# Performance work log

Hardware: AMD Instinct MI355X
Metric: run time of the kernel (lower is better)

## Reference

```python
import jax, jax.numpy as jnp
import numpy as np

# ---- static config (LCNN wirenet) ----
K = 128            # fixed junction count per type (n_dyn_junc // n_type)
N_PTS0 = 32
N_PTS1 = 8
SCALE = N_PTS0 // N_PTS1   # maxpool1d kernel/stride = 4
DIM_LOI = 128
DIM_FC = 1024
FEATURE_DIM = 8
USE_COOD = 0.0
USE_SLOP = 0.0
HW = 128
B = 2
# static u<v pair indices (torch: meshgrid -> c = u < v), P = K*(K-1)/2
IU_np, IV_np = np.triu_indices(K, k=1)
P = IU_np.shape[0]
IU = jnp.asarray(IU_np, jnp.int32)
IV = jnp.asarray(IV_np, jnp.int32)
LAMBDA = jnp.linspace(0.0, 1.0, N_PTS0)[:, None]  # [32,1]


def setup_inputs() -> dict:
    key = jax.random.key(0)
    ks = jax.random.split(key, 8)
    inputs = jax.random.normal(ks[0], (B, 5, HW, HW), jnp.float32)
    features = jax.random.normal(ks[1], (B, 256, HW, HW), jnp.float32)
    fc1_w = jax.random.normal(ks[2], (DIM_LOI, 256), jnp.float32) * 0.05
    fc1_b = jnp.zeros((DIM_LOI,), jnp.float32)
    d_in = DIM_LOI * N_PTS1 + FEATURE_DIM  # 1032
    w1 = jax.random.normal(ks[3], (d_in, DIM_FC), jnp.float32) * 0.03
    b1 = jnp.zeros((DIM_FC,), jnp.float32)
    w2 = jax.random.normal(ks[4], (DIM_FC, DIM_FC), jnp.float32) * 0.03
    b2 = jnp.zeros((DIM_FC,), jnp.float32)
    w3 = jax.random.normal(ks[5], (DIM_FC, 1), jnp.float32) * 0.03
    b3 = jnp.zeros((1,), jnp.float32)
    return dict(inputs=inputs, features=features, fc1_w=fc1_w, fc1_b=fc1_b,
                w1=w1, b1=b1, w2=w2, b2=b2, w3=w3, b3=b3)


def _nms(a):
    # a: [1,H,W]; 3x3 max-pool NMS, keep only local maxima
    ap = jax.lax.reduce_window(a, -jnp.inf, jax.lax.max, (1, 3, 3), (1, 1, 1), 'SAME')
    return a * (a == ap).astype(a.dtype)


def _sample_lines(jmap, joff):
    # jmap: [1,H,W], joff: [1,2,H,W]  (inference path: dummy junc/Lpos)
    n_type = 1
    jm = _nms(jmap).reshape(n_type, -1)            # [1, HW*HW]
    jo = joff.reshape(n_type, 2, -1)
    score, index = jax.lax.top_k(jm, K)            # [1,K]
    y = (index // HW).astype(jnp.float32) + jnp.take_along_axis(jo[:, 0], index, 1) + 0.5
    x = (index % HW).astype(jnp.float32) + jnp.take_along_axis(jo[:, 1], index, 1) + 0.5
    xy = jnp.stack([y, x], -1)                     # [1,K,2]
    # inference dummies: junc=zeros(1,2), jtyp=zeros(1), Lpos=zeros(2,2)
    junc = jnp.zeros((1, 2), jnp.float32)
    jtyp = jnp.zeros((1,), jnp.int32)
    dist = jnp.sum((xy[:, :, None, :] - junc) ** 2, -1)  # [1,K,1]
    cost = jnp.min(dist, -1)
    match = jnp.argmin(dist, -1).astype(jnp.int32)       # [1,K]
    Njunc = 1
    match = jnp.where(jtyp[match] != jnp.arange(n_type, dtype=jnp.int32)[:, None], Njunc, match)
    match = jnp.where(cost > 1.5 * 1.5, Njunc, match).reshape(-1)  # [K]
    up, vp = match[IU], match[IV]
    Lpos = jnp.zeros((2, 2), jnp.float32)
    label = Lpos[up, vp]                           # [P]
    xyf = xy.reshape(n_type * K, 2)
    xyu, xyv = xyf[IU], xyf[IV]                    # [P,2]
    u2v = xyu - xyv
    u2v = u2v / jnp.clip(jnp.sqrt(jnp.sum(u2v ** 2, -1, keepdims=True)), 1e-6)
    feat = jnp.concatenate([
        xyu / HW * USE_COOD, xyv / HW * USE_COOD, u2v * USE_SLOP,
        (IU[:, None] > K).astype(jnp.float32), (IV[:, None] > K).astype(jnp.float32)], 1)  # [P,8]
    line = jnp.stack([xyu, xyv], 1)                # [P,2,2]
    return line, label, feat


def _loi_pool(xfeat, line):
    # xfeat: [C,H,W], line: [P,2,2] -> [P,C,N_PTS1]
    p = line[:, 0:1, :] * LAMBDA + line[:, 1:2, :] * (1.0 - LAMBDA) - 0.5  # [P,32,2]
    p = p.reshape(-1, 2)
    px, py = p[:, 0], p[:, 1]
    px0 = jnp.clip(jnp.floor(px), 0, HW - 1)
    py0 = jnp.clip(jnp.floor(py), 0, HW - 1)
    px1 = jnp.clip(px0 + 1, 0, HW - 1)
    py1 = jnp.clip(py0 + 1, 0, HW - 1)
    px0l = px0.astype(jnp.int32); py0l = py0.astype(jnp.int32)
    px1l = px1.astype(jnp.int32); py1l = py1.astype(jnp.int32)
    xp = (xfeat[:, px0l, py0l] * (px1 - px) * (py1 - py)
          + xfeat[:, px1l, py0l] * (px - px0) * (py1 - py)
          + xfeat[:, px0l, py1l] * (px1 - px) * (py - py0)
          + xfeat[:, px1l, py1l] * (px - px0) * (py - py0))  # [C, P*32]
    xp = xp.reshape(DIM_LOI, -1, N_PTS0).transpose(1, 0, 2)  # [P,C,32]
    # MaxPool1d(kernel=4, stride=4)
    return xp.reshape(xp.shape[0], DIM_LOI, N_PTS1, SCALE).max(-1)  # [P,C,8]


def _forward(inputs, features, fc1_w, fc1_b, w1, b1, w2, b2, w3, b3):
    b, _, r, c = inputs.shape
    out = jnp.transpose(inputs, (1, 0, 2, 3))       # [5,B,H,W]
    jmap_logits = out[0:2].reshape(1, 2, b, r, c)
    joff_logits = out[3:5].reshape(1, 2, b, r, c)
    jmap = jax.nn.softmax(jnp.transpose(jmap_logits, (2, 0, 1, 3, 4)), axis=2)[:, :, 1]  # [B,1,H,W]
    joff = jax.nn.sigmoid(jnp.transpose(joff_logits, (2, 0, 1, 3, 4))) - 0.5             # [B,1,2,H,W]
    # fc1: 1x1 conv 256 -> dim_loi
    xf = jnp.einsum('bchw,dc->bdhw', features, fc1_w) + fc1_b[None, :, None, None]
    lines, labels, feats = jax.vmap(_sample_lines)(jmap, joff)   # [B,P,2,2],[B,P],[B,P,8]
    # sample_lines runs under torch.no_grad()
    lines = jax.lax.stop_gradient(lines)
    labels = jax.lax.stop_gradient(labels)
    feats = jax.lax.stop_gradient(feats)
    xp = jax.vmap(_loi_pool)(xf, lines)             # [B,P,C,8]
    xv = xp.reshape(-1, N_PTS1 * DIM_LOI)           # [B*P, 1024] (C-major then pts)
    xv = jnp.concatenate([xv, feats.reshape(-1, FEATURE_DIM)], 1)  # [B*P, 1032]
    h = jax.nn.relu(xv @ w1 + b1)
    h = jax.nn.relu(h @ w2 + b2)
    scores = (h @ w3 + b3).reshape(-1)              # [B*P]
    return scores, labels.reshape(-1), lines


def reference(inputs, features, fc1_w, fc1_b, w1, b1, w2, b2, w3, b3):
    return _forward(inputs, features, fc1_w, fc1_b, w1, b1, w2, b2, w3, b3)
```

## Files before the change

kernel.cpp:

```cpp
#include <hip/hip_runtime.h>
#include <hip/hip_bf16.h>
#include <math.h>

#define HW 128
#define NPIX 16384
#define KTOP 128
#define PPAIR 8128
#define NB 2
#define DIMLOI 128
#define NROWS (NB*PPAIR)
#define MPAD 16384

typedef __bf16 bf16x8 __attribute__((ext_vector_type(8)));
typedef float floatx4 __attribute__((ext_vector_type(4)));
typedef float floatx8 __attribute__((ext_vector_type(8)));

__device__ __forceinline__ unsigned long long mk_key(float v, int idx) {
    return ((unsigned long long)__float_as_uint(v) << 32) |
           (unsigned long long)(0xFFFFFFFFu - (unsigned)idx);
}

__device__ __forceinline__ unsigned long long shfl_xor_u64(unsigned long long x, int m) {
    unsigned lo = (unsigned)x, hi = (unsigned)(x >> 32);
    lo = __shfl_xor(lo, m);
    hi = __shfl_xor(hi, m);
    return ((unsigned long long)hi << 32) | lo;
}

__device__ __forceinline__ void bitonic_stage(unsigned long long V[4], int lane, int j, int k) {
    if (j >= 64) {
        int qm = j >> 6;
        #pragma unroll
        for (int q = 0; q < 4; q++) {
            int p = q ^ qm;
            if (p > q) {
                int i = q * 64 + lane;
                bool desc = ((i & k) == 0);
                unsigned long long a = V[q], b = V[p];
                unsigned long long hi = a > b ? a : b, lo = a > b ? b : a;
                V[q] = desc ? hi : lo;
                V[p] = desc ? lo : hi;
            }
        }
    } else {
        #pragma unroll
        for (int q = 0; q < 4; q++) {
            int i = q * 64 + lane;
            unsigned long long p = shfl_xor_u64(V[q], j);
            bool lower = (lane & j) == 0;
            bool desc = ((i & k) == 0);
            bool keepmax = (desc == lower);
            unsigned long long mx = V[q] > p ? V[q] : p;
            unsigned long long mn = V[q] > p ? p : V[q];
            V[q] = keepmax ? mx : mn;
        }
    }
}

__device__ __forceinline__ void sort256_desc(unsigned long long V[4], int lane) {
    #pragma unroll
    for (int k = 2; k <= 256; k <<= 1)
        #pragma unroll
        for (int j = k >> 1; j >= 1; j >>= 1)
            bitonic_stage(V, lane, j, k);
}

__device__ __forceinline__ void merge256_desc(unsigned long long V[4], int lane) {
    #pragma unroll
    for (int j = 128; j >= 1; j >>= 1)
        bitonic_stage(V, lane, j, 256);
}

__global__ __launch_bounds__(256) void nms_sort_kernel(const float* __restrict__ inp,
                                                       unsigned long long* __restrict__ tkeys) {
    __shared__ float jm[10 * HW];
    __shared__ unsigned long long cand[256];
    __shared__ int scnt;
    int blk = blockIdx.x;
    int b   = blockIdx.y;
    int tid = threadIdx.x, lane = tid & 63;
    int r0  = blk * 8;
    int rlo = (r0 > 0) ? r0 - 1 : 0;
    int rhi = (r0 + 8 < HW) ? r0 + 8 : HW - 1;
    int nrows = rhi - rlo + 1;

    for (int i = tid; i < nrows * HW; i += 256) {
        int pix = rlo * HW + i;
        float l0 = inp[((long)b * 5 + 0) * NPIX + pix];
        float l1 = inp[((long)b * 5 + 1) * NPIX + pix];
        float m = fmaxf(l0, l1);
        float e0 = expf(l0 - m), e1 = expf(l1 - m);
        jm[i] = e1 / (e0 + e1);
    }
    cand[tid] = 0ull;
    if (tid == 0) scnt = 0;
    __syncthreads();

    #pragma unroll
    for (int i = 0; i < 4; i++) {
        int pl = i * 256 + tid;
        int r = r0 + (pl >> 7), c = pl & 127;
        float v = jm[(r - rlo) * HW + c];
        float m = v;
        for (int dr = -1; dr <= 1; dr++) {
            int rr = r + dr;
            if (rr < 0 || rr >= HW) continue;
            for (int dc = -1; dc <= 1; dc++) {
                int cc = c + dc;
                if (cc < 0 || cc >= HW) continue;
                m = fmaxf(m, jm[(rr - rlo) * HW + cc]);
            }
        }
        float nv = (v == m) ? v : 0.f;
        bool has = (nv > 0.f);
        unsigned long long mask = __ballot(has);
        int n = __popcll(mask);
        int wbase = 0;
        if (lane == 0 && n) wbase = atomicAdd(&scnt, n);
        wbase = __shfl(wbase, 0);
        if (has) {
            int pos = wbase + __popcll(mask & ((1ull << lane) - 1ull));
            if (pos < 256) cand[pos] = mk_key(nv, r * HW + c);
        }
    }
    __syncthreads();
    if (blk == 0 && tid < 128 && tid >= scnt) cand[tid] = mk_key(0.f, tid);
    __syncthreads();

    if (tid < 64) {
        unsigned long long V[4];
        #pragma unroll
        for (int q = 0; q < 4; q++) V[q] = cand[q * 64 + lane];
        sort256_desc(V, lane);
        #pragma unroll
        for (int q = 0; q < 2; q++)
            tkeys[((long)b * 16 + blk) * 128 + q * 64 + lane] = V[q];
    }
}

__global__ __launch_bounds__(512) void topk_merge_kernel(const unsigned long long* __restrict__ tkeys,
                                                         const float* __restrict__ inp,
                                                         float* __restrict__ xy) {
    __shared__ unsigned long long Lb[16 * 128];
    __shared__ unsigned long long Mb[8 * 128];
    int b = blockIdx.x;
    int tid = threadIdx.x, w = tid >> 6, lane = tid & 63;
    for (int i = tid; i < 16 * 128; i += 512) Lb[i] = tkeys[(long)b * 2048 + i];
    __syncthreads();

    unsigned long long* src = Lb;
    unsigned long long* dst = Mb;
    for (int nact = 8; nact >= 1; nact >>= 1) {
        unsigned long long V[4];
        if (w < nact) {
            #pragma unroll
            for (int q = 0; q < 2; q++) V[q] = src[(2 * w) * 128 + q * 64 + lane];
            #pragma unroll
            for (int q = 2; q < 4; q++) {
                int t = (q - 2) * 64 + lane;
                V[q] = src[(2 * w + 1) * 128 + 127 - t];
            }
            merge256_desc(V, lane);
        }
        __syncthreads();
        if (w < nact) {
            #pragma unroll
            for (int q = 0; q < 2; q++) dst[w * 128 + q * 64 + lane] = V[q];
        }
        __syncthreads();
        unsigned long long* tmp = src; src = dst; dst = tmp;
    }

    if (tid < KTOP) {
        unsigned long long key = src[tid];
        int wi = (int)(0xFFFFFFFFu - (unsigned)(key & 0xFFFFFFFFull));
        int row = wi >> 7, col = wi & 127;
        float l3 = inp[((long)b * 5 + 3) * NPIX + wi];
        float l4 = inp[((long)b * 5 + 4) * NPIX + wi];
        float joy = 1.f / (1.f + expf(-l3)) - 0.5f;
        float jox = 1.f / (1.f + expf(-l4)) - 0.5f;
        xy[(b * KTOP + tid) * 2 + 0] = (float)row + joy + 0.5f;
        xy[(b * KTOP + tid) * 2 + 1] = (float)col + jox + 0.5f;
    }
}

__device__ __forceinline__ void pair_uv(int p, int& u, int& v) {
    int uu = (int)((255.0 - sqrt(65025.0 - 8.0 * (double)p)) * 0.5);
    if (uu < 0) uu = 0;
    while (uu * (255 - uu) / 2 > p) uu--;
    while ((uu + 1) * (255 - (uu + 1)) / 2 <= p) uu++;
    u = uu;
    v = uu + 1 + (p - uu * (255 - uu) / 2);
}

__global__ void lines_kernel(const float* __restrict__ xy, float* __restrict__ out) {
    int r = blockIdx.x * 256 + threadIdx.x;
    if (r >= NROWS) return;
    int b = r / PPAIR, p = r % PPAIR;
    int u, v; pair_uv(p, u, v);
    float yu = xy[(b * KTOP + u) * 2 + 0], xu = xy[(b * KTOP + u) * 2 + 1];
    float yv = xy[(b * KTOP + v) * 2 + 0], xv = xy[(b * KTOP + v) * 2 + 1];
    float* lines = out + 2 * NROWS;
    long base = (long)r * 4;
    lines[base + 0] = yu; lines[base + 1] = xu;
    lines[base + 2] = yv; lines[base + 3] = xv;
    out[NROWS + r] = 0.f;
}

__global__ void prep_weights(const float* __restrict__ w1, const float* __restrict__ w2,
                             const float* __restrict__ fc1w,
                             __hip_bfloat16* __restrict__ w1t, __hip_bfloat16* __restrict__ w2t,
                             __hip_bfloat16* __restrict__ fc1wb) {
    int z = blockIdx.z;
    int tx = threadIdx.x & 31, ty = threadIdx.x >> 5;
    if (z < 2) {
        const float* W = z ? w2 : w1;
        __hip_bfloat16* Wt = z ? w2t : w1t;
        __shared__ float t[32][33];
        int k0 = blockIdx.x * 32, n0 = blockIdx.y * 32;
        #pragma unroll
        for (int i = 0; i < 32; i += 8)
            t[ty + i][tx] = W[(long)(k0 + ty + i) * 1024 + n0 + tx];
        __syncthreads();
        #pragma unroll
        for (int i = 0; i < 32; i += 8)
            Wt[(long)(n0 + ty + i) * 1024 + k0 + tx] = __float2bfloat16(t[tx][ty + i]);
    } else {
        if (blockIdx.x < 4 && blockIdx.y < 8) {
            int r0 = blockIdx.x * 32, c0 = blockIdx.y * 32;
            #pragma unroll
            for (int i = 0; i < 32; i += 8) {
                long idx = (long)(r0 + ty + i) * 256 + c0 + tx;
                fc1wb[idx] = __float2bfloat16(fc1w[idx]);
            }
        }
    }
}

__device__ __forceinline__ void gload_lds16(const void* g, void* l) {
    __builtin_amdgcn_global_load_lds(
        (const __attribute__((address_space(1))) void*)g,
        (__attribute__((address_space(3))) void*)l, 16, 0, 0);
}

#define SA 264

__global__ __launch_bounds__(256) void xf_fused_kernel(
    const float* __restrict__ features, const __hip_bfloat16* __restrict__ fc1wb,
    const float* __restrict__ bias, __hip_bfloat16* __restrict__ C0) {
    __shared__ __align__(16) __bf16 A_lds[128 * SA];
    __shared__ __align__(16) unsigned short B_lds[128 * 32 * 8];
    int tid = threadIdx.x;
    int lane = tid & 63, wid = tid >> 6;
    int wr = wid >> 1, wc = wid & 1;
    int b = blockIdx.z;
    long pix0 = (long)blockIdx.x * 128;

    #pragma unroll
    for (int it = 0; it < 16; it++) {
        int slot = it * 256 + tid;
        int r = slot >> 5, s = slot & 31;
        int ss = s ^ (r & 7);
        gload_lds16(fc1wb + (size_t)r * 256 + ss * 8,
                    (char*)B_lds + (size_t)(it * 4096 + wid * 1024));
    }
    {
        int c = tid;
        const float* src = features + ((long)b * 256 + c) * NPIX + pix0;
        #pragma unroll
        for (int p4 = 0; p4 < 32; p4++) {
            floatx4 v = *(const floatx4*)(src + p4 * 4);
            #pragma unroll
            for (int e = 0; e < 4; e++)
                A_lds[(p4 * 4 + e) * SA + c] = (__bf16)v[e];
        }
    }
    __syncthreads();

    floatx4 acc[4][4];
    #pragma unroll
    for (int i = 0; i < 4; i++)
        #pragma unroll
        for (int j = 0; j < 4; j++) acc[i][j] = (floatx4){0.f, 0.f, 0.f, 0.f};

    int r15 = lane & 15;
    #pragma unroll
    for (int ks = 0; ks < 8; ks++) {
        int s = (lane >> 4) + ks * 4;
        bf16x8 af[4], bfr[4];
        #pragma unroll
        for (int mi = 0; mi < 4; mi++) {
            int R = wr * 64 + mi * 16 + r15;
            af[mi] = *(const bf16x8*)&A_lds[R * SA + s * 8];
        }
        #pragma unroll
        for (int ni = 0; ni < 4; ni++) {
            int Rn = wc * 64 + ni * 16 + r15;
            bfr[ni] = *(const bf16x8*)&B_lds[(size_t)Rn * 256 + ((s ^ (Rn & 7)) << 3)];
        }
        #pragma unroll
        for (int mi = 0; mi < 4; mi++)
            #pragma unroll
            for (int ni = 0; ni < 4; ni++)
                acc[mi][ni] = __builtin_amdgcn_mfma_f32_16x16x32_bf16(
                    af[mi], bfr[ni], acc[mi][ni], 0, 0, 0);
    }

    __hip_bfloat16* C = C0 + (long)b * NPIX * DIMLOI;
    #pragma unroll
    for (int ni = 0; ni < 4; ni++) {
        long c = wc * 64 + ni * 16 + r15;
        float bv = bias[c];
        #pragma unroll
        for (int mi = 0; mi < 4; mi++) {
            long rbase = pix0 + wr * 64 + mi * 16 + (lane >> 4) * 4;
            #pragma unroll
            for (int q = 0; q < 4; q++)
                C[(rbase + q) * (long)DIMLOI + c] = __float2bfloat16(acc[mi][ni][q] + bv);
        }
    }
}

#define BM 128
#define BN 128
#define BKK 64

template <bool SCORE>
__global__ __launch_bounds__(256) void gemm_mfma(
    const __hip_bfloat16* __restrict__ A, const __hip_bfloat16* __restrict__ Bt,
    const float* __restrict__ bias, __hip_bfloat16* __restrict__ C,
    int M, int N, int Kd,
    const float* __restrict__ w3, float* __restrict__ slab) {
    int bid = blockIdx.x;
    int xcd = bid & 7, j = bid >> 3;
    int mtpx = (M / BM) >> 3;
    int mt = xcd * mtpx + (j >> 3);
    int nt = j & 7;
    long row0 = (long)mt * BM, col0 = (long)nt * BN;

    __shared__ __align__(16) unsigned short As[BM * BKK];
    __shared__ __align__(16) unsigned short Bs[BN * BKK];
    int tid = threadIdx.x;
    int lane = tid & 63, wid = tid >> 6;
    int wr = wid >> 1, wc = wid & 1;

    floatx4 acc[4][4];
    #pragma unroll
    for (int i = 0; i < 4; i++)
        #pragma unroll
        for (int jj = 0; jj < 4; jj++) acc[i][jj] = (floatx4){0.f, 0.f, 0.f, 0.f};

    for (int k0 = 0; k0 < Kd; k0 += BKK) {
        #pragma unroll
        for (int it = 0; it < 4; it++) {
            int slot = wid * 256 + it * 64 + lane;
            int r = slot >> 3, s = slot & 7;
            int ss = s ^ (r & 7);
            gload_lds16(A + (row0 + r) * Kd + k0 + ss * 8,
                        (char*)As + (size_t)(wid * 4096 + it * 1024));
        }
        #pragma unroll
        for (int it = 0; it < 4; it++) {
            int slot = wid * 256 + it * 64 + lane;
            int r = slot >> 3, s = slot & 7;
            int ss = s ^ (r & 7);
            gload_lds16(Bt + (col0 + r) * Kd + k0 + ss * 8,
                        (char*)Bs + (size_t)(wid * 4096 + it * 1024));
        }
        __syncthreads();
        #pragma unroll
        for (int ks = 0; ks < 2; ks++) {
            bf16x8 af[4], bfr[4];
            int s = (lane >> 4) + ks * 4;
            #pragma unroll
            for (int mi = 0; mi < 4; mi++) {
                int R = wr * 64 + mi * 16 + (lane & 15);
                af[mi] = *(const bf16x8*)&As[R * BKK + ((s ^ (R & 7)) << 3)];
            }
            #pragma unroll
            for (int ni = 0; ni < 4; ni++) {
                int Rn = wc * 64 + ni * 16 + (lane & 15);
                bfr[ni] = *(const bf16x8*)&Bs[Rn * BKK + ((s ^ (Rn & 7)) << 3)];
            }
            #pragma unroll
            for (int mi = 0; mi < 4; mi++)
                #pragma unroll
                for (int ni = 0; ni < 4; ni++)
                    acc[mi][ni] = __builtin_amdgcn_mfma_f32_16x16x32_bf16(
                        af[mi], bfr[ni], acc[mi][ni], 0, 0, 0);
        }
        __syncthreads();
    }

    if constexpr (SCORE) {
        int ntile = (int)(col0 / BN);
        #pragma unroll
        for (int mi = 0; mi < 4; mi++) {
            #pragma unroll
            for (int q = 0; q < 4; q++) {
                float p = 0.f;
                #pragma unroll
                for (int ni = 0; ni < 4; ni++) {
                    long c = col0 + wc * 64 + ni * 16 + (lane & 15);
                    float v = fmaxf(acc[mi][ni][q] + bias[c], 0.f);
                    p += v * w3[c];
                }
                #pragma unroll
                for (int off = 1; off < 16; off <<= 1) p += __shfl_xor(p, off);
                if ((lane & 15) == 0) {
                    long row = row0 + wr * 64 + mi * 16 + (lane >> 4) * 4 + q;
                    slab[(long)(ntile * 2 + wc) * MPAD + row] = p;
                }
            }
        }
    } else {
        #pragma unroll
        for (int ni = 0; ni < 4; ni++) {
            long c = col0 + wc * 64 + ni * 16 + (lane & 15);
            float bv = bias[c];
            #pragma unroll
            for (int mi = 0; mi < 4; mi++) {
                long rbase = row0 + wr * 64 + mi * 16 + (lane >> 4) * 4;
                #pragma unroll
                for (int q = 0; q < 4; q++) {
                    float v = fmaxf(acc[mi][ni][q] + bv, 0.f);
                    C[(rbase + q) * (long)N + c] = __float2bfloat16(v);
                }
            }
        }
    }
}

__global__ void score_reduce_kernel(const float* __restrict__ slab, const float* __restrict__ b3,
                                    float* __restrict__ out) {
    int r = blockIdx.x * 256 + threadIdx.x;
    if (r >= NROWS) return;
    float s = b3[0];
    #pragma unroll
    for (int i = 0; i < 16; i++) s += slab[(long)i * MPAD + r];
    out[r] = s;
}

__global__ __launch_bounds__(256) void loi_sample_kernel(
    const __hip_bfloat16* __restrict__ xf, const float* __restrict__ xy,
    __hip_bfloat16* __restrict__ xp) {
    __shared__ int md[16 * 32 * 8];
    int tid = threadIdx.x;
    int bid = blockIdx.x;
    int swz = (bid & 7) * 128 + (bid >> 3);
    int rbase = swz * 16;

    {
        int pt0 = tid * 2;
        int sub = pt0 >> 5;
        int r = rbase + sub;
        int rm = (r < NROWS) ? r : NROWS - 1;
        int b = rm / PPAIR, p = rm % PPAIR;
        int u, v; pair_uv(p, u, v);
        float yu = xy[(b * KTOP + u) * 2 + 0], xu = xy[(b * KTOP + u) * 2 + 1];
        float yv = xy[(b * KTOP + v) * 2 + 0], xv = xy[(b * KTOP + v) * 2 + 1];
        #pragma unroll
        for (int pp = 0; pp < 2; pp++) {
            int t = (pt0 + pp) & 31;
            float lam = (float)t * (1.0f / 31.0f);
            float px = yu * lam + yv * (1.f - lam) - 0.5f;
            float py = xu * lam + xv * (1.f - lam) - 0.5f;
            float px0 = fminf(fmaxf(floorf(px), 0.f), 127.f);
            float py0 = fminf(fmaxf(floorf(py), 0.f), 127.f);
            float px1 = fminf(px0 + 1.f, 127.f);
            float py1 = fminf(py0 + 1.f, 127.f);
            int ix0 = (int)px0, iy0 = (int)py0, ix1 = (int)px1, iy1 = (int)py1;
            int base = (pt0 + pp) * 8;
            md[base + 0] = (ix0 * HW + iy0) * (DIMLOI * 2);
            md[base + 1] = (ix1 * HW + iy0) * (DIMLOI * 2);
            md[base + 2] = (ix0 * HW + iy1) * (DIMLOI * 2);
            md[base + 3] = (ix1 * HW + iy1) * (DIMLOI * 2);
            md[base + 4] = __float_as_int((px1 - px) * (py1 - py));
            md[base + 5] = __float_as_int((px - px0) * (py1 - py));
            md[base + 6] = __float_as_int((px1 - px) * (py - py0));
            md[base + 7] = __float_as_int((px - px0) * (py - py0));
        }
    }
    __syncthreads();

    int sub2 = tid >> 4, o = tid & 15;
    int r = rbase + sub2;
    int rm = (r < NROWS) ? r : NROWS - 1;
    int b = rm / PPAIR;
    const char* xfb = (const char*)(xf + (long)b * NPIX * DIMLOI) + o * 16;
    floatx8 mx[8];
    #pragma unroll
    for (int q = 0; q < 8; q++)
        #pragma unroll
        for (int e = 0; e < 8; e++) mx[q][e] = -INFINITY;
    #pragma unroll
    for (int tt = 0; tt < 32; tt++) {
        const int* m = &md[(sub2 * 32 + tt) * 8];
        bf16x8 v00 = *(const bf16x8*)(xfb + m[0]);
        bf16x8 v10 = *(const bf16x8*)(xfb + m[1]);
        bf16x8 v01 = *(const bf16x8*)(xfb + m[2]);
        bf16x8 v11 = *(const bf16x8*)(xfb + m[3]);
        float w00 = __int_as_float(m[4]), w10 = __int_as_float(m[5]);
        float w01 = __int_as_float(m[6]), w11 = __int_as_float(m[7]);
        floatx8 s;
        #pragma unroll
        for (int e = 0; e < 8; e++)
            s[e] = (float)v00[e] * w00 + (float)v10[e] * w10 +
                   (float)v01[e] * w01 + (float)v11[e] * w11;
        mx[tt >> 2] = __builtin_elementwise_max(mx[tt >> 2], s);
    }
    __hip_bfloat16* rowp = xp + (long)r * 1024 + o * 64;
    #pragma unroll
    for (int e = 0; e < 8; e++) {
        bf16x8 outv;
        #pragma unroll
        for (int q = 0; q < 8; q++) outv[q] = (__bf16)mx[q][e];
        *(bf16x8*)(rowp + e * 8) = outv;
    }
}

extern "C" void kernel_launch(void* const* d_in, const int* in_sizes, int n_in,
                              void* d_out, int out_size, void* d_ws, size_t ws_size,
                              hipStream_t stream) {
    const float* inputs   = (const float*)d_in[0];
    const float* features = (const float*)d_in[1];
    const float* fc1_w    = (const float*)d_in[2];
    const float* fc1_b    = (const float*)d_in[3];
    const float* w1       = (const float*)d_in[4];
    const float* b1       = (const float*)d_in[5];
    const float* w2       = (const float*)d_in[6];
    const float* b2       = (const float*)d_in[7];
    const float* w3       = (const float*)d_in[8];
    const float* b3       = (const float*)d_in[9];
    float* out = (float*)d_out;
    float* ws  = (float*)d_ws;

    float* xy   = ws + 65536;
    __hip_bfloat16* xfb16 = (__hip_bfloat16*)(ws + 66048);
    __hip_bfloat16* xp    = (__hip_bfloat16*)(ws + 4260352);
    __hip_bfloat16* h1    = (__hip_bfloat16*)(ws + 12648960);
    float* slab           = ws + 21037568;
    __hip_bfloat16* w1t   = (__hip_bfloat16*)(ws + 21299712);
    __hip_bfloat16* w2t   = (__hip_bfloat16*)(ws + 21824000);
    __hip_bfloat16* fc1wb = (__hip_bfloat16*)(ws + 22348288);
    unsigned long long* tkeys = (unsigned long long*)(ws + 22364672);

    prep_weights<<<dim3(32, 32, 3), 256, 0, stream>>>(w1, w2, fc1_w, w1t, w2t, fc1wb);

    nms_sort_kernel<<<dim3(16, NB), 256, 0, stream>>>(inputs, tkeys);
    topk_merge_kernel<<<NB, 512, 0, stream>>>(tkeys, inputs, xy);
    lines_kernel<<<(NROWS + 255) / 256, 256, 0, stream>>>(xy, out);

    xf_fused_kernel<<<dim3(NPIX / 128, 1, NB), 256, 0, stream>>>(
        features, fc1wb, fc1_b, xfb16);

    loi_sample_kernel<<<MPAD / 16, 256, 0, stream>>>(xfb16, xy, xp);

    gemm_mfma<false><<<(MPAD / BM) * 8, 256, 0, stream>>>(
        xp, w1t, b1, h1, MPAD, 1024, 1024, nullptr, nullptr);
    gemm_mfma<true><<<(MPAD / BM) * 8, 256, 0, stream>>>(
        h1, w2t, b2, nullptr, MPAD, 1024, 1024, w3, slab);
    score_reduce_kernel<<<(NROWS + 255) / 256, 256, 0, stream>>>(slab, b3, out);
}
```

Measured before the change: 167.5 us.

## Rewrite MLP GEMMs as 256x256-tile 8-wave kernels with double-buffered LDS pipeline

The two MLP GEMMs move from 128x128 tiles with 4 waves to 256x256 tiles with 8 waves. LDS staging is now double-buffered, with the A and B loads issued one and two k-steps ahead and interleaved with MFMA phases under explicit vmcnt waits, barriers and setprio. The goal is to hide global-to-LDS latency and cut global traffic per FLOP through more operand reuse. In exchange the kernel uses more registers and LDS, launches only 256 blocks, and hard-codes M/N/K to 1024, so occupancy and load balance may suffer.

```diff
diff --git a/kernel.cpp b/kernel.cpp
--- a/kernel.cpp
+++ b/kernel.cpp
@@ -321,110 +321,136 @@
     }
 }
 
-#define BM 128
-#define BN 128
-#define BKK 64
+#define NT16 16
 
 template <bool SCORE>
-__global__ __launch_bounds__(256) void gemm_mfma(
+__global__ __launch_bounds__(512, 2) void gemm_mlp8(
     const __hip_bfloat16* __restrict__ A, const __hip_bfloat16* __restrict__ Bt,
     const float* __restrict__ bias, __hip_bfloat16* __restrict__ C,
-    int M, int N, int Kd,
     const float* __restrict__ w3, float* __restrict__ slab) {
+    __shared__ __align__(128) unsigned short As[2][2][128][8][8];
+    __shared__ __align__(128) unsigned short Bs[2][2][128][8][8];
+    int tid = threadIdx.x;
+    int lane = tid & 63, wid = tid >> 6;
+    int wr = wid >> 2, wn = wid & 3;
+    int r15 = lane & 15, s4 = lane >> 4;
     int bid = blockIdx.x;
     int xcd = bid & 7, j = bid >> 3;
-    int mtpx = (M / BM) >> 3;
-    int mt = xcd * mtpx + (j >> 3);
-    int nt = j & 7;
-    long row0 = (long)mt * BM, col0 = (long)nt * BN;
-
-    __shared__ __align__(16) unsigned short As[BM * BKK];
-    __shared__ __align__(16) unsigned short Bs[BN * BKK];
-    int tid = threadIdx.x;
-    int lane = tid & 63, wid = tid >> 6;
-    int wr = wid >> 1, wc = wid & 1;
-
-    floatx4 acc[4][4];
-    #pragma unroll
-    for (int i = 0; i < 4; i++)
-        #pragma unroll
-        for (int jj = 0; jj < 4; jj++) acc[i][jj] = (floatx4){0.f, 0.f, 0.f, 0.f};
-
-    for (int k0 = 0; k0 < Kd; k0 += BKK) {
-        #pragma unroll
-        for (int it = 0; it < 4; it++) {
-            int slot = wid * 256 + it * 64 + lane;
-            int r = slot >> 3, s = slot & 7;
-            int ss = s ^ (r & 7);
-            gload_lds16(A + (row0 + r) * Kd + k0 + ss * 8,
-                        (char*)As + (size_t)(wid * 4096 + it * 1024));
-        }
-        #pragma unroll
-        for (int it = 0; it < 4; it++) {
-            int slot = wid * 256 + it * 64 + lane;
-            int r = slot >> 3, s = slot & 7;
-            int ss = s ^ (r & 7);
-            gload_lds16(Bt + (col0 + r) * Kd + k0 + ss * 8,
-                        (char*)Bs + (size_t)(wid * 4096 + it * 1024));
-        }
-        __syncthreads();
-        #pragma unroll
-        for (int ks = 0; ks < 2; ks++) {
-            bf16x8 af[4], bfr[4];
-            int s = (lane >> 4) + ks * 4;
-            #pragma unroll
-            for (int mi = 0; mi < 4; mi++) {
-                int R = wr * 64 + mi * 16 + (lane & 15);
-                af[mi] = *(const bf16x8*)&As[R * BKK + ((s ^ (R & 7)) << 3)];
-            }
-            #pragma unroll
-            for (int ni = 0; ni < 4; ni++) {
-                int Rn = wc * 64 + ni * 16 + (lane & 15);
-                bfr[ni] = *(const bf16x8*)&Bs[Rn * BKK + ((s ^ (Rn & 7)) << 3)];
-            }
-            #pragma unroll
-            for (int mi = 0; mi < 4; mi++)
+    int mt = xcd * 8 + (j >> 2), nt = j & 3;
+    long row0 = (long)mt * 256, col0 = (long)nt * 256;
+
+    auto stageA = [&](int tk, int h) {
+        int bf = tk & 1;
+        #pragma unroll
+        for (int it = 0; it < 2; it++) {
+            int sl = it * 512 + tid;
+            int r = sl >> 3, s = sl & 7;
+            gload_lds16(A + (row0 + h * 128 + r) * 1024 + tk * 64 + ((s ^ (r & 7)) << 3),
+                        (char*)&As[bf][h][0][0][0] + (size_t)sl * 16);
+        }
+    };
+    auto stageB = [&](int tk, int h) {
+        int bf = tk & 1;
+        #pragma unroll
+        for (int it = 0; it < 2; it++) {
+            int sl = it * 512 + tid;
+            int r = sl >> 3, s = sl & 7;
+            gload_lds16(Bt + (col0 + h * 128 + r) * 1024 + tk * 64 + ((s ^ (r & 7)) << 3),
+                        (char*)&Bs[bf][h][0][0][0] + (size_t)sl * 16);
+        }
+    };
+
+    floatx4 acc[8][4];
+    #pragma unroll
+    for (int mi = 0; mi < 8; mi++)
+        #pragma unroll
+        for (int nf = 0; nf < 4; nf++) acc[mi][nf] = (floatx4){0.f, 0.f, 0.f, 0.f};
+
+    stageA(0, 0); stageA(0, 1); stageB(0, 0); stageB(0, 1); stageB(1, 0); stageB(1, 1);
+    asm volatile("s_waitcnt vmcnt(4)" ::: "memory");
+    __builtin_amdgcn_s_barrier();
+
+    for (int t = 0; t < NT16; t++) {
+        int bf = t & 1;
+        bf16x8 bfr[4][2];
+        #pragma unroll
+        for (int p = 0; p < 4; p++) {
+            if (p == 0) {
                 #pragma unroll
-                for (int ni = 0; ni < 4; ni++)
-                    acc[mi][ni] = __builtin_amdgcn_mfma_f32_16x16x32_bf16(
-                        af[mi], bfr[ni], acc[mi][ni], 0, 0, 0);
-        }
-        __syncthreads();
+                for (int nf = 0; nf < 4; nf++)
+                    #pragma unroll
+                    for (int ks = 0; ks < 2; ks++) {
+                        int Rb = wn * 64 + nf * 16 + r15;
+                        int rh = Rb & 127;
+                        bfr[nf][ks] = *(const bf16x8*)&Bs[bf][Rb >> 7][rh][(ks * 4 + s4) ^ (rh & 7)][0];
+                    }
+            }
+            bf16x8 af[2][2];
+            #pragma unroll
+            for (int m = 0; m < 2; m++)
+                #pragma unroll
+                for (int ks = 0; ks < 2; ks++) {
+                    int rh = (2 * p + m) * 16 + r15;
+                    af[m][ks] = *(const bf16x8*)&As[bf][wr][rh][(ks * 4 + s4) ^ (rh & 7)][0];
+                }
+            if (p == 0) { if (t + 1 < NT16) stageA(t + 1, 0); }
+            else if (p == 1) { if (t + 1 < NT16) stageA(t + 1, 1); }
+            else if (p == 2) { if (t + 2 < NT16) stageB(t + 2, 0); }
+            else             { if (t + 2 < NT16) stageB(t + 2, 1); }
+            if (p == 3) {
+                if (t < NT16 - 2) { asm volatile("s_waitcnt vmcnt(4)" ::: "memory"); }
+                else              { asm volatile("s_waitcnt vmcnt(0)" ::: "memory"); }
+            }
+            __builtin_amdgcn_s_barrier();
+            asm volatile("s_waitcnt lgkmcnt(0)" ::: "memory");
+            __builtin_amdgcn_sched_barrier(0);
+            __builtin_amdgcn_s_setprio(1);
+            #pragma unroll
+            for (int m = 0; m < 2; m++)
+                #pragma unroll
+                for (int nf = 0; nf < 4; nf++)
+                    #pragma unroll
+                    for (int ks = 0; ks < 2; ks++)
+                        acc[2 * p + m][nf] = __builtin_amdgcn_mfma_f32_16x16x32_bf16(
+                            af[m][ks], bfr[nf][ks], acc[2 * p + m][nf], 0, 0, 0);
+            __builtin_amdgcn_s_setprio(0);
+            __builtin_amdgcn_s_barrier();
+        }
     }
 
     if constexpr (SCORE) {
-        int ntile = (int)(col0 / BN);
-        #pragma unroll
-        for (int mi = 0; mi < 4; mi++) {
+        int slot = nt * 4 + wn;
+        #pragma unroll
+        for (int mi = 0; mi < 8; mi++) {
             #pragma unroll
             for (int q = 0; q < 4; q++) {
                 float p = 0.f;
                 #pragma unroll
-                for (int ni = 0; ni < 4; ni++) {
-                    long c = col0 + wc * 64 + ni * 16 + (lane & 15);
-                    float v = fmaxf(acc[mi][ni][q] + bias[c], 0.f);
+                for (int nf = 0; nf < 4; nf++) {
+                    long c = col0 + wn * 64 + nf * 16 + r15;
+                    float v = fmaxf(acc[mi][nf][q] + bias[c], 0.f);
                     p += v * w3[c];
                 }
                 #pragma unroll
                 for (int off = 1; off < 16; off <<= 1) p += __shfl_xor(p, off);
-                if ((lane & 15) == 0) {
-                    long row = row0 + wr * 64 + mi * 16 + (lane >> 4) * 4 + q;
-                    slab[(long)(ntile * 2 + wc) * MPAD + row] = p;
+                if (r15 == 0) {
+                    long row = row0 + wr * 128 + mi * 16 + s4 * 4 + q;
+                    slab[(long)slot * MPAD + row] = p;
                 }
             }
         }
     } else {
         #pragma unroll
-        for (int ni = 0; ni < 4; ni++) {
-            long c = col0 + wc * 64 + ni * 16 + (lane & 15);
+        for (int nf = 0; nf < 4; nf++) {
+            long c = col0 + wn * 64 + nf * 16 + r15;
             float bv = bias[c];
             #pragma unroll
-            for (int mi = 0; mi < 4; mi++) {
-                long rbase = row0 + wr * 64 + mi * 16 + (lane >> 4) * 4;
+            for (int mi = 0; mi < 8; mi++) {
+                long rbase = row0 + wr * 128 + mi * 16 + s4 * 4;
                 #pragma unroll
                 for (int q = 0; q < 4; q++) {
-                    float v = fmaxf(acc[mi][ni][q] + bv, 0.f);
-                    C[(rbase + q) * (long)N + c] = __float2bfloat16(v);
+                    float v = fmaxf(acc[mi][nf][q] + bv, 0.f);
+                    C[(rbase + q) * 1024L + c] = __float2bfloat16(v);
                 }
             }
         }
@@ -556,9 +582,7 @@
 
     loi_sample_kernel<<<MPAD / 16, 256, 0, stream>>>(xfb16, xy, xp);
 
-    gemm_mfma<false><<<(MPAD / BM) * 8, 256, 0, stream>>>(
-        xp, w1t, b1, h1, MPAD, 1024, 1024, nullptr, nullptr);
-    gemm_mfma<true><<<(MPAD / BM) * 8, 256, 0, stream>>>(
-        h1, w2t, b2, nullptr, MPAD, 1024, 1024, w3, slab);
+    gemm_mlp8<false><<<256, 512, 0, stream>>>(xp, w1t, b1, h1, nullptr, nullptr);
+    gemm_mlp8<true><<<256, 512, 0, stream>>>(h1, w2t, b2, nullptr, w3, slab);
     score_reduce_kernel<<<(NROWS + 255) / 256, 256, 0, stream>>>(slab, b3, out);
 }
```

Result: faster. 163.6 us (-2.3%).
